# Kernel tuning notes

Measured on AMD Instinct MI355X. Metric: run time of the kernel, lower is better.

Reference implementation:

```python
import math
import jax, jax.numpy as jnp
import numpy as np

B, T, C = 2, 2048, 1024
H, N1, N2, N3 = 16, 6, 4, 6
HD = C // H  # 64


def setup_inputs() -> dict:
    key = jax.random.key(0)
    k1, k2, k3 = jax.random.split(key, 3)
    return {
        "x": jax.random.normal(k1, (B, T, C), jnp.float32),
        "qkv_w": jax.random.normal(k2, (3 * C, C), jnp.float32) * (C ** -0.5),
        "proj_w": jax.random.normal(k3, (C, C), jnp.float32) * (C ** -0.5),
        "proj_b": jnp.zeros((C,), jnp.float32),
        "curvature": jnp.ones((1, N2, 1, 1), jnp.float32),
    }


def _rotary(T_, hd, dtype):
    inv_freq = 1.0 / (10000.0 ** (jnp.arange(0, hd, 2, dtype=jnp.float32) / hd))
    freqs = jnp.outer(jnp.arange(T_, dtype=jnp.float32), inv_freq)  # [T, hd/2]
    return jnp.cos(freqs)[None, :, None, :].astype(dtype), jnp.sin(freqs)[None, :, None, :].astype(dtype)


def _apply_rot(x, cos, sin):
    x1, x2 = x[..., : x.shape[-1] // 2], x[..., x.shape[-1] // 2 :]
    return jnp.concatenate([x1 * cos + x2 * sin, -x1 * sin + x2 * cos], axis=-1).astype(x.dtype)


def _causal_bias(L, S, dtype):
    mask = jnp.triu(jnp.ones((L, S), bool), k=1)
    return jnp.where(mask, jnp.asarray(-jnp.inf, dtype), jnp.asarray(0.0, dtype))


def _sdpa(q, k, v, scale):
    # q,k,v: [B,h,T,hd]
    scores = jnp.einsum("bhtd,bhsd->bhts", q, k) * scale + _causal_bias(q.shape[-2], k.shape[-2], q.dtype)
    return jnp.einsum("bhts,bhsd->bhtd", jax.nn.softmax(scores, axis=-1), v)


def _hyp_attn(q, k, v, curv):
    # Lorentz-model hyperbolic attention. project(x,k) = [sqrt(1/k+||x||^2), x];
    # d(u,v) = sqrt(1/k) * arccosh(-k * <u,v>_L), <u,v>_L = -u0 v0 + <u_s, v_s>.
    eps = 1e-6
    tq = jnp.sqrt(1.0 / curv + jnp.sum(q * q, axis=-1, keepdims=True))  # [B,h,T,1]
    tk = jnp.sqrt(1.0 / curv + jnp.sum(k * k, axis=-1, keepdims=True))  # [B,h,S,1]
    inner = jnp.einsum("bhtd,bhsd->bhts", q, k) - tq * jnp.swapaxes(tk, -1, -2)  # Lorentz inner [B,h,T,S]
    arg = jnp.maximum(-curv * inner, 1.0 + 1e-7)
    dis = jnp.sqrt(1.0 / curv) * jnp.arccosh(arg)
    scores = 1.0 / (eps + dis) + _causal_bias(q.shape[-2], k.shape[-2], q.dtype)
    return jnp.einsum("bhts,bhsd->bhtd", jax.nn.softmax(scores, axis=-1), v)


def reference(x, qkv_w, proj_w, proj_b, curvature):
    Bx, Tx, Cx = x.shape
    qkv = x @ qkv_w.T  # [B,T,3C]
    q, k, v = jnp.split(qkv, 3, axis=-1)
    q = q.reshape(Bx, Tx, H, HD)
    k = k.reshape(Bx, Tx, H, HD)
    v = v.reshape(Bx, Tx, H, HD)
    cos, sin = _rotary(Tx, HD, x.dtype)
    q = _apply_rot(q, cos, sin)
    k = _apply_rot(k, cos, sin)
    # -> [B,H,T,hd]
    q, k, v = (jnp.swapaxes(t, 1, 2) for t in (q, k, v))
    outs = []
    # euclidean heads
    outs.append(_sdpa(q[:, :N1], k[:, :N1], v[:, :N1], 1.0 / math.sqrt(HD)))
    # hyperbolic heads
    outs.append(_hyp_attn(q[:, N1 : N1 + N2], k[:, N1 : N1 + N2], v[:, N1 : N1 + N2], curvature))
    # spherical heads (cosine-sim attention, scale = sqrt(head_dim))
    qn = q[:, N1 + N2 :] / jnp.maximum(jnp.linalg.norm(q[:, N1 + N2 :], axis=-1, keepdims=True), 1e-12)
    kn = k[:, N1 + N2 :] / jnp.maximum(jnp.linalg.norm(k[:, N1 + N2 :], axis=-1, keepdims=True), 1e-12)
    outs.append(_sdpa(qn, kn, v[:, N1 + N2 :], math.sqrt(HD)))
    y = jnp.concatenate(outs, axis=1)  # [B,H,T,hd]
    y = jnp.swapaxes(y, 1, 2).reshape(Bx, Tx, Cx)
    return y @ proj_w.T + proj_b
```

## Files before the change

kernel.cpp:

```cpp
#include <hip/hip_runtime.h>
#include <stdint.h>
#include <math.h>


typedef __bf16 bf16x8 __attribute__((ext_vector_type(8)));
typedef float f32x4 __attribute__((ext_vector_type(4)));

static __device__ __forceinline__ float bf2f(unsigned short u) {
  union { unsigned int i; float f; } v; v.i = ((unsigned int)u) << 16; return v.f;
}
static __device__ __forceinline__ unsigned short f2bf(float f) {
  union { float f; unsigned int i; } v; v.f = f;
  unsigned int x = v.i;
  x += 0x7fffu + ((x >> 16) & 1u);
  return (unsigned short)(x >> 16);
}

static __device__ __forceinline__ void async_copy16(const void* gsrc, void* ldst) {
  auto* lp = reinterpret_cast<__attribute__((address_space(3))) unsigned int*>(
      reinterpret_cast<uintptr_t>(ldst));
  auto* gp = reinterpret_cast<const __attribute__((address_space(1))) unsigned int*>(
      reinterpret_cast<uintptr_t>(gsrc));
  __builtin_amdgcn_global_load_lds(gp, lp, 16, 0, 0);
}

template <int PAT>
__global__ __launch_bounds__(256) void split2(const float* __restrict__ in,
                                              unsigned short* __restrict__ out) {
  const int row = blockIdx.x;
  const int kq = threadIdx.x * 4;
  const f32x4 x = *(const f32x4*)(in + (size_t)row * 1024 + kq);
  unsigned short hi[4], lo[4];
#pragma unroll
  for (int i = 0; i < 4; ++i) {
    hi[i] = f2bf(x[i]);
    lo[i] = f2bf(x[i] - bf2f(hi[i]));
  }
  uint2 uh, ul;
  uh.x = (unsigned)hi[0] | ((unsigned)hi[1] << 16);
  uh.y = (unsigned)hi[2] | ((unsigned)hi[3] << 16);
  ul.x = (unsigned)lo[0] | ((unsigned)lo[1] << 16);
  ul.y = (unsigned)lo[2] | ((unsigned)lo[3] << 16);
  unsigned short* op = out + (size_t)row * 2048 + kq;
  *(uint2*)(op)        = uh;
  *(uint2*)(op + 1024) = PAT ? uh : ul;
}

template <int HASBIAS>
__global__ __launch_bounds__(256) void gemm_bt(
    const unsigned short* __restrict__ A, const unsigned short* __restrict__ Bm,
    float* __restrict__ C, const float* __restrict__ bias, int N_, int K_) {
  alignas(16) __shared__ unsigned short smA[128 * 64];
  alignas(16) __shared__ unsigned short smB[128 * 64];
  const int tid = threadIdx.x;
  const int lane = tid & 63;
  const int wv = tid >> 6;
  const int wm = wv >> 1, wn = wv & 1;
  const long m0 = (long)blockIdx.y * 128, n0 = (long)blockIdx.x * 128;

  const f32x4 zero4 = {0.f, 0.f, 0.f, 0.f};
  f32x4 acc[4][4];
#pragma unroll
  for (int i = 0; i < 4; ++i)
#pragma unroll
    for (int j = 0; j < 4; ++j) acc[i][j] = zero4;

  int mrow[4], gg[4];
#pragma unroll
  for (int w = 0; w < 4; ++w) {
    int c = w * 256 + tid;
    mrow[w] = c >> 3;
    gg[w] = (c & 7) ^ ((c >> 3) & 7);
  }

  const int kTiles = K_ >> 6;
  for (int kt = 0; kt < kTiles; ++kt) {
    if (kt) __syncthreads();
    const int kb = kt << 6;
#pragma unroll
    for (int w = 0; w < 4; ++w) {
      const int c = w * 256 + tid;
      async_copy16(A + (size_t)(m0 + mrow[w]) * K_ + kb + gg[w] * 8,
                   (char*)smA + c * 16);
      async_copy16(Bm + (size_t)(n0 + mrow[w]) * K_ + kb + gg[w] * 8,
                   (char*)smB + c * 16);
    }
    __syncthreads();
#pragma unroll
    for (int ks = 0; ks < 2; ++ks) {
      bf16x8 af[4], bg[4];
#pragma unroll
      for (int i = 0; i < 4; ++i) {
        const int ra = wm * 64 + i * 16 + (lane & 15);
        const int ga = (ks * 4 + (lane >> 4)) ^ (ra & 7);
        af[i] = *(const bf16x8*)((const char*)smA + ra * 128 + ga * 16);
        const int rb = wn * 64 + i * 16 + (lane & 15);
        const int gb2 = (ks * 4 + (lane >> 4)) ^ (rb & 7);
        bg[i] = *(const bf16x8*)((const char*)smB + rb * 128 + gb2 * 16);
      }
#pragma unroll
      for (int i = 0; i < 4; ++i)
#pragma unroll
        for (int j = 0; j < 4; ++j)
          acc[i][j] = __builtin_amdgcn_mfma_f32_16x16x32_bf16(af[i], bg[j], acc[i][j], 0, 0, 0);
    }
  }

  const int r0 = wm * 64 + (lane >> 4) * 4;
  const int c0 = wn * 64 + (lane & 15);
#pragma unroll
  for (int j = 0; j < 4; ++j) {
    const long col = n0 + c0 + j * 16;
    float bv = 0.f;
    if (HASBIAS) bv = bias[col];
#pragma unroll
    for (int i = 0; i < 4; ++i) {
#pragma unroll
      for (int r = 0; r < 4; ++r) {
        const long row = m0 + r0 + i * 16 + r;
        C[row * N_ + col] = acc[i][j][r] + bv;
      }
    }
  }
}

__global__ __launch_bounds__(256) void prep(
    const float* __restrict__ qkvf, unsigned short* __restrict__ Q2,
    unsigned short* __restrict__ K2, unsigned short* __restrict__ V2,
    float* __restrict__ qq, float* __restrict__ kk, const float* __restrict__ curvg) {
  __shared__ unsigned short Vl[64 * 66];
  const int tid = threadIdx.x;
  const int zz = blockIdx.x;
  const int ttile = zz & 31, bh = zz >> 5;
  const int b = bh >> 4, h = bh & 15;
  const int t0 = ttile * 64;
  const int tr = tid >> 2, seg = tid & 3;
  const int t = t0 + tr;
  const float* src = qkvf + ((size_t)(b * 2048 + t)) * 3072 + h * 64 + seg * 16;

  float qv[16], kv[16], vv[16];
#pragma unroll
  for (int c = 0; c < 4; ++c) {
    const f32x4 a  = *(const f32x4*)(src + c * 4);
    const f32x4 bb = *(const f32x4*)(src + 1024 + c * 4);
    const f32x4 cc = *(const f32x4*)(src + 2048 + c * 4);
#pragma unroll
    for (int e = 0; e < 4; ++e) { qv[c*4+e] = a[e]; kv[c*4+e] = bb[e]; vv[c*4+e] = cc[e]; }
  }
  float qr[16], kr[16];
#pragma unroll
  for (int e = 0; e < 16; ++e) {
    const int d = seg * 16 + e;
    const int i = d & 31;
    const float invf = exp2f(-0.41524101186109286f * (float)i);
    float sn, cs;
    sincosf((float)t * invf, &sn, &cs);
    const float qo = __shfl_xor(qv[e], 2, 64);
    const float ko = __shfl_xor(kv[e], 2, 64);
    qr[e] = (d < 32) ? (qv[e] * cs + qo * sn) : (qv[e] * cs - qo * sn);
    kr[e] = (d < 32) ? (kv[e] * cs + ko * sn) : (kv[e] * cs - ko * sn);
  }
  float sq = 0.f, sk = 0.f;
#pragma unroll
  for (int e = 0; e < 16; ++e) { sq += qr[e] * qr[e]; sk += kr[e] * kr[e]; }
  sq += __shfl_xor(sq, 1, 64); sq += __shfl_xor(sq, 2, 64);
  sk += __shfl_xor(sk, 1, 64); sk += __shfl_xor(sk, 2, 64);
  float qscale = 0.125f * 1.4426950408889634f;
  if (h >= 10) {
    const float rq = 1.0f / fmaxf(sqrtf(sq), 1e-12f);
    const float rk = 1.0f / fmaxf(sqrtf(sk), 1e-12f);
#pragma unroll
    for (int e = 0; e < 16; ++e) { qr[e] *= rq; kr[e] *= rk; }
    qscale = 8.0f * 1.4426950408889634f;
  } else if (h >= 6) {
    qscale = 1.0f;
  }
#pragma unroll
  for (int e = 0; e < 16; ++e) qr[e] *= qscale;
  if (seg == 0) {
    const int idx = b * 32768 + h * 2048 + t;
    float oq = sq, ok = sk;
    if (h >= 6 && h < 10) {
      const float invc = 1.0f / curvg[h - 6];
      oq = sqrtf(invc + sq);
      ok = sqrtf(invc + sk);
    }
    qq[idx] = oq;
    kk[idx] = ok;
  }
  const int st = seg >> 1;
  const int quadA = (seg * 2) & 3, quadB = (seg * 2 + 1) & 3;
  {
    unsigned int wh[8], wl[8];
#pragma unroll
    for (int p = 0; p < 8; ++p) {
      unsigned short h0 = f2bf(qr[2*p]), h1 = f2bf(qr[2*p+1]);
      unsigned short l0 = f2bf(qr[2*p] - bf2f(h0)), l1 = f2bf(qr[2*p+1] - bf2f(h1));
      wh[p] = (unsigned)h0 | ((unsigned)h1 << 16);
      wl[p] = (unsigned)l0 | ((unsigned)l1 << 16);
    }
    const int qi = (t >> 4) & 1, c15q = t & 15;
    unsigned short* qs = Q2 + ((size_t)bh * 64 + (t >> 5)) * 4096;
    const int fh = ((qi * 2 + st) * 2 + 0) * 512, fl = fh + 512;
    *(uint4*)(qs + fh + quadA * 128 + c15q * 8) = uint4{wh[0], wh[1], wh[2], wh[3]};
    *(uint4*)(qs + fh + quadB * 128 + c15q * 8) = uint4{wh[4], wh[5], wh[6], wh[7]};
    *(uint4*)(qs + fl + quadA * 128 + c15q * 8) = uint4{wl[0], wl[1], wl[2], wl[3]};
    *(uint4*)(qs + fl + quadB * 128 + c15q * 8) = uint4{wl[4], wl[5], wl[6], wl[7]};
#pragma unroll
    for (int p = 0; p < 8; ++p) {
      unsigned short h0 = f2bf(kr[2*p]), h1 = f2bf(kr[2*p+1]);
      wh[p] = (unsigned)h0 | ((unsigned)h1 << 16);
    }
    const int kj = (tr >> 4) & 3, c15k = tr & 15;
    unsigned short* ks = K2 + ((size_t)bh * 32 + ttile) * 4096;
    const int gh = (st * 4 + kj) * 512;
    *(uint4*)(ks + gh + quadA * 128 + c15k * 8) = uint4{wh[0], wh[1], wh[2], wh[3]};
    *(uint4*)(ks + gh + quadB * 128 + c15k * 8) = uint4{wh[4], wh[5], wh[6], wh[7]};
  }
#pragma unroll
  for (int e = 0; e < 16; ++e) Vl[(seg * 16 + e) * 66 + tr] = f2bf(vv[e]);
  __syncthreads();
  {
    const int d = tid >> 2, tch = (tid & 3) * 16;
    unsigned int wv2[8];
#pragma unroll
    for (int p = 0; p < 8; ++p) {
      const unsigned short a0 = Vl[d * 66 + tch + 2*p];
      const unsigned short a1 = Vl[d * 66 + tch + 2*p + 1];
      wv2[p] = (unsigned)a0 | ((unsigned)a1 << 16);
    }
    const int dj = d >> 4, c15v = d & 15;
    const int ks2 = tch >> 5;
    const int qvA = (tch >> 3) & 3, qvB = ((tch >> 3) + 1) & 3;
    unsigned short* vs = V2 + ((size_t)bh * 32 + ttile) * 4096 + (ks2 * 4 + dj) * 512;
    *(uint4*)(vs + qvA * 128 + c15v * 8) = uint4{wv2[0], wv2[1], wv2[2], wv2[3]};
    *(uint4*)(vs + qvB * 128 + c15v * 8) = uint4{wv2[4], wv2[5], wv2[6], wv2[7]};
  }
}

__global__ __launch_bounds__(256, 2) void attn_part(
    const unsigned short* __restrict__ Q2, const unsigned short* __restrict__ K2,
    const unsigned short* __restrict__ V2, const float* __restrict__ tqq,
    const float* __restrict__ tkk, const float* __restrict__ curvg,
    float* __restrict__ part) {
  alignas(16) __shared__ unsigned short Pl[4][32 * 64];
  const int tid = threadIdx.x;
  const int lane = tid & 63;
  const int wv = tid >> 6;
  unsigned short* Pw = &Pl[wv][0];
  const int quad = lane >> 4, c15 = lane & 15;
  const int z = blockIdx.x * 4 + wv;
  const int bh = z / 160;
  const int u = 159 - (z - bh * 160);
  int qw, ch;
  if (u < 16)      { qw = u; ch = 0; }
  else if (u < 48) { qw = 16 + ((u - 16) >> 1); ch = (u - 16) & 1; }
  else if (u < 96) { const int s2 = u - 48; const int q3 = s2 / 3; qw = 32 + q3; ch = s2 - 3 * q3; }
  else             { const int s2 = u - 96; qw = 48 + (s2 >> 2); ch = s2 & 3; }
  const int h = bh & 15;
  const int geom = (h < 6) ? 0 : ((h < 10) ? 1 : 2);
  const int qrow0 = qw * 32;
  const f32x4 zero4 = {0.f, 0.f, 0.f, 0.f};

  const unsigned short* qbase = Q2 + ((size_t)bh * 64 + qw) * 4096;
  bf16x8 qh[2][2], ql[2][2];
#pragma unroll
  for (int qi = 0; qi < 2; ++qi)
#pragma unroll
    for (int st = 0; st < 2; ++st) {
      const int f = ((qi * 2 + st) * 2) * 512 + lane * 8;
      qh[qi][st] = *(const bf16x8*)(qbase + f);
      ql[qi][st] = *(const bf16x8*)(qbase + f + 512);
    }

  float curv = 1.f, sic = 1.f;
  const float Moff = 4.0f;
  f32x4 tq4[2] = {zero4, zero4};
  if (geom == 1) {
    curv = curvg[h - 6];
    sic = sqrtf(1.0f / curv);
#pragma unroll
    for (int qi = 0; qi < 2; ++qi)
      tq4[qi] = *(const f32x4*)(tqq + bh * 2048 + qrow0 + qi * 16 + quad * 4);
  }

  const __bf16 one_b = (__bf16)1.0f;
  const bf16x8 ones = {one_b, one_b, one_b, one_b, one_b, one_b, one_b, one_b};

  f32x4 o[2][4];
  f32x4 ol[2] = {zero4, zero4};
#pragma unroll
  for (int qi = 0; qi < 2; ++qi)
#pragma unroll
    for (int dj = 0; dj < 4; ++dj) o[qi][dj] = zero4;

  const int nkt = (qw >> 1) + 1;
  const int ktB = ch * 8;
  const int ktE = (ktB + 8 < nkt) ? (ktB + 8) : nkt;
  for (int kt = ktB; kt < ktE; ++kt) {
    const int kb = kt * 64;
    const unsigned short* kbase = K2 + ((size_t)bh * 32 + kt) * 4096;
    const unsigned short* vbase = V2 + ((size_t)bh * 32 + kt) * 4096;

    bf16x8 kf[2][4], vf[2][4];
#pragma unroll
    for (int st = 0; st < 2; ++st)
#pragma unroll
      for (int kj = 0; kj < 4; ++kj)
        kf[st][kj] = *(const bf16x8*)(kbase + (st * 4 + kj) * 512 + lane * 8);
#pragma unroll
    for (int ks2 = 0; ks2 < 2; ++ks2)
#pragma unroll
      for (int dj = 0; dj < 4; ++dj)
        vf[ks2][dj] = *(const bf16x8*)(vbase + (ks2 * 4 + dj) * 512 + lane * 8);
    float tkf[4];
    if (geom == 1) {
#pragma unroll
      for (int kj = 0; kj < 4; ++kj)
        tkf[kj] = tkk[bh * 2048 + kb + kj * 16 + c15];
    }

    f32x4 s[2][4];
#pragma unroll
    for (int qi = 0; qi < 2; ++qi)
#pragma unroll
      for (int kj = 0; kj < 4; ++kj) s[qi][kj] = zero4;
    __builtin_amdgcn_s_setprio(1);
#pragma unroll
    for (int st = 0; st < 2; ++st) {
#pragma unroll
      for (int kj = 0; kj < 4; ++kj) {
#pragma unroll
        for (int qi = 0; qi < 2; ++qi) {
          s[qi][kj] = __builtin_amdgcn_mfma_f32_16x16x32_bf16(qh[qi][st], kf[st][kj], s[qi][kj], 0, 0, 0);
          s[qi][kj] = __builtin_amdgcn_mfma_f32_16x16x32_bf16(ql[qi][st], kf[st][kj], s[qi][kj], 0, 0, 0);
        }
      }
    }
    __builtin_amdgcn_s_setprio(0);

    const bool needmask = (kt == nkt - 1);
#pragma unroll
    for (int qi = 0; qi < 2; ++qi) {
      const int qbaserow = qrow0 + qi * 16 + quad * 4;
#pragma unroll
      for (int kj = 0; kj < 4; ++kj) {
        const int skey = kj * 16 + c15;
        const int key = kb + skey;
        const f32x4 d4 = s[qi][kj];
        f32x4 p;
        if (geom == 1) {
          const float tk = tkf[kj];
#pragma unroll
          for (int r = 0; r < 4; ++r) {
            const float a = fmaxf(curv * (tq4[qi][r] * tk - d4[r]), 1.0f + 1e-7f);
            const float dis = sic * __logf(a + sqrtf(a * a - 1.0f));
            p[r] = __expf(__builtin_amdgcn_rcpf(1e-6f + dis) - Moff);
          }
        } else {
#pragma unroll
          for (int r = 0; r < 4; ++r) p[r] = exp2f(d4[r]);
        }
        if (needmask) {
#pragma unroll
          for (int r = 0; r < 4; ++r)
            if (key > qbaserow + r) p[r] = 0.0f;
        }
#pragma unroll
        for (int r = 0; r < 4; ++r) {
          union { float f; unsigned u2; } pv; pv.f = p[r];
          const int row = qi * 16 + quad * 4 + r;
          const int g = (skey >> 3) ^ (row & 7);
          Pw[row * 64 + g * 8 + (skey & 7)] = (unsigned short)(pv.u2 >> 16);
        }
      }
    }

    __builtin_amdgcn_s_setprio(1);
#pragma unroll
    for (int ks2 = 0; ks2 < 2; ++ks2) {
      bf16x8 av[2];
#pragma unroll
      for (int qi = 0; qi < 2; ++qi) {
        const int m = qi * 16 + c15;
        const int g = (ks2 * 4 + quad) ^ (m & 7);
        av[qi] = *(const bf16x8*)(Pw + m * 64 + g * 8);
        ol[qi] = __builtin_amdgcn_mfma_f32_16x16x32_bf16(av[qi], ones, ol[qi], 0, 0, 0);
      }
#pragma unroll
      for (int dj = 0; dj < 4; ++dj) {
#pragma unroll
        for (int qi = 0; qi < 2; ++qi)
          o[qi][dj] = __builtin_amdgcn_mfma_f32_16x16x32_bf16(av[qi], vf[ks2][dj], o[qi][dj], 0, 0, 0);
      }
    }
    __builtin_amdgcn_s_setprio(0);
  }

  float* slot = part + (size_t)(bh * 160 + u) * 2112;
#pragma unroll
  for (int qi = 0; qi < 2; ++qi)
#pragma unroll
    for (int dj = 0; dj < 4; ++dj)
      *(f32x4*)(slot + (qi * 4 + dj) * 256 + lane * 4) = o[qi][dj];
  if (c15 == 0) {
#pragma unroll
    for (int qi = 0; qi < 2; ++qi)
      *(f32x4*)(slot + 2048 + qi * 16 + quad * 4) = ol[qi];
  }
}

__global__ __launch_bounds__(256) void attn_reduce(
    const float* __restrict__ part, unsigned short* __restrict__ Ay) {
  __shared__ float Ol[4][32 * 65];
  const int tid = threadIdx.x;
  const int lane = tid & 63;
  const int wv = tid >> 6;
  float* Olw = &Ol[wv][0];
  const int quad = lane >> 4, c15 = lane & 15;
  const int z = blockIdx.x * 4 + wv, bh = z & 31, qw = 63 - (z >> 5);
  const int b = bh >> 4, h = bh & 15;
  const int G = qw >> 4;
  const int base = qw + 8 * G * (G - 1) + (qw & 15) * G;
  const float* slot0 = part + (size_t)(bh * 160 + base) * 2112;

  const f32x4 zero4 = {0.f, 0.f, 0.f, 0.f};
  f32x4 o[8];
  f32x4 l4[2] = {zero4, zero4};
#pragma unroll
  for (int i = 0; i < 8; ++i) o[i] = zero4;
  for (int chv = 0; chv <= G; ++chv) {
    const float* sl = slot0 + chv * 2112;
#pragma unroll
    for (int i = 0; i < 8; ++i) o[i] += *(const f32x4*)(sl + i * 256 + lane * 4);
#pragma unroll
    for (int qi = 0; qi < 2; ++qi)
      l4[qi] += *(const f32x4*)(sl + 2048 + qi * 16 + quad * 4);
  }
#pragma unroll
  for (int qi = 0; qi < 2; ++qi) {
    f32x4 invl;
#pragma unroll
    for (int r = 0; r < 4; ++r) invl[r] = __builtin_amdgcn_rcpf(l4[qi][r]);
#pragma unroll
    for (int dj = 0; dj < 4; ++dj) {
      const f32x4 val = o[qi * 4 + dj] * invl;
#pragma unroll
      for (int r = 0; r < 4; ++r)
        Olw[(qi * 16 + quad * 4 + r) * 65 + dj * 16 + c15] = val[r];
    }
  }
  __syncthreads();
  const int row = lane >> 1, half = lane & 1;
  const float* rp = Olw + row * 65 + half * 32;
  unsigned int uh[16], ul2[16];
#pragma unroll
  for (int p = 0; p < 16; ++p) {
    const float v0 = rp[2 * p], v1 = rp[2 * p + 1];
    const unsigned short h0 = f2bf(v0), h1 = f2bf(v1);
    const unsigned short g0 = f2bf(v0 - bf2f(h0)), g1 = f2bf(v1 - bf2f(h1));
    uh[p] = (unsigned)h0 | ((unsigned)h1 << 16);
    ul2[p] = (unsigned)g0 | ((unsigned)g1 << 16);
  }
  unsigned short* yp = Ay + ((size_t)(b * 2048 + qw * 32 + row)) * 2048 + h * 64 + half * 32;
#pragma unroll
  for (int c = 0; c < 4; ++c) {
    *(uint4*)(yp + 8 * c)        = uint4{uh[4*c], uh[4*c+1], uh[4*c+2], uh[4*c+3]};
    *(uint4*)(yp + 1024 + 8 * c) = uint4{ul2[4*c], ul2[4*c+1], ul2[4*c+2], ul2[4*c+3]};
  }
}

extern "C" void kernel_launch(void* const* d_in, const int* in_sizes, int n_in,
                              void* d_out, int out_size, void* d_ws, size_t ws_size,
                              hipStream_t stream) {
  const float* x      = (const float*)d_in[0];
  const float* qkv_w  = (const float*)d_in[1];
  const float* proj_w = (const float*)d_in[2];
  const float* proj_b = (const float*)d_in[3];
  const float* curvature = (const float*)d_in[4];
  float* out = (float*)d_out;

  char* ws = (char*)d_ws;
  unsigned short* AX   = (unsigned short*)ws;
  unsigned short* BW   = (unsigned short*)(ws + 16777216);
  float*          QKVF = (float*)(ws + 33554432);
  unsigned short* Q2   = (unsigned short*)ws;
  unsigned short* K2   = (unsigned short*)(ws + 16777216);
  unsigned short* V2   = (unsigned short*)(ws + 25165824);
  float*          PART = (float*)(ws + 33554432);
  unsigned short* BPW  = (unsigned short*)(ws + 76808192);
  unsigned short* AY   = (unsigned short*)ws;
  float*          QQ   = (float*)(ws + 94371840);
  float*          KK   = (float*)(ws + 94633984);

  split2<0><<<4096, 256, 0, stream>>>(x, AX);
  split2<1><<<3072, 256, 0, stream>>>(qkv_w, BW);

  gemm_bt<0><<<dim3(24, 32), 256, 0, stream>>>(AX, BW, QKVF, nullptr, 3072, 2048);

  prep<<<1024, 256, 0, stream>>>(QKVF, Q2, K2, V2, QQ, KK, curvature);

  split2<1><<<1024, 256, 0, stream>>>(proj_w, BPW);

  attn_part<<<1280, 256, 0, stream>>>(Q2, K2, V2, QQ, KK, curvature, PART);

  attn_reduce<<<512, 256, 0, stream>>>(PART, AY);

  gemm_bt<1><<<dim3(8, 32), 256, 0, stream>>>(AY, BPW, out, proj_b, 1024, 2048);
}
```

Baseline: 286.7 us.

## Transpose score MFMAs and pass P via ds_bpermute instead of LDS

Swaps the MFMA operand order so scores come out transposed (keys along rows, queries along lanes). The probability tile can then be packed into registers and redistributed with ds_bpermute as the B operand of the PV MFMA, instead of a scatter-store to shared memory and a read-back. Downstream indexing for tq/tk, the causal mask, row-sum output and the reduce kernel's layout are adjusted to match. It removes the per-wave LDS P buffer and its strided 2-byte stores, but adds 16 bpermutes and selects per tile.

After: 285.2 us. About the same (-0.5%).

```diff
diff --git a/kernel.cpp b/kernel.cpp
--- a/kernel.cpp
+++ b/kernel.cpp
@@ -243,11 +243,9 @@
     const unsigned short* __restrict__ V2, const float* __restrict__ tqq,
     const float* __restrict__ tkk, const float* __restrict__ curvg,
     float* __restrict__ part) {
-  alignas(16) __shared__ unsigned short Pl[4][32 * 64];
   const int tid = threadIdx.x;
   const int lane = tid & 63;
   const int wv = tid >> 6;
-  unsigned short* Pw = &Pl[wv][0];
   const int quad = lane >> 4, c15 = lane & 15;
   const int z = blockIdx.x * 4 + wv;
   const int bh = z / 160;
@@ -275,17 +273,21 @@
 
   float curv = 1.f, sic = 1.f;
   const float Moff = 4.0f;
-  f32x4 tq4[2] = {zero4, zero4};
+  float tqs[2] = {0.f, 0.f};
   if (geom == 1) {
     curv = curvg[h - 6];
     sic = sqrtf(1.0f / curv);
 #pragma unroll
     for (int qi = 0; qi < 2; ++qi)
-      tq4[qi] = *(const f32x4*)(tqq + bh * 2048 + qrow0 + qi * 16 + quad * 4);
+      tqs[qi] = tqq[bh * 2048 + qrow0 + qi * 16 + c15];
   }
 
   const __bf16 one_b = (__bf16)1.0f;
   const bf16x8 ones = {one_b, one_b, one_b, one_b, one_b, one_b, one_b, one_b};
+
+  const int iA = ((quad & 1) * 32 + c15) * 4;
+  const int iB = iA + 64;
+  const bool hiq = (quad >= 2);
 
   f32x4 o[2][4];
   f32x4 ol[2] = {zero4, zero4};
@@ -313,11 +315,11 @@
 #pragma unroll
       for (int dj = 0; dj < 4; ++dj)
         vf[ks2][dj] = *(const bf16x8*)(vbase + (ks2 * 4 + dj) * 512 + lane * 8);
-    float tkf[4];
+    f32x4 tk4[4];
     if (geom == 1) {
 #pragma unroll
       for (int kj = 0; kj < 4; ++kj)
-        tkf[kj] = tkk[bh * 2048 + kb + kj * 16 + c15];
+        tk4[kj] = *(const f32x4*)(tkk + bh * 2048 + kb + kj * 16 + quad * 4);
     }
 
     f32x4 s[2][4];
@@ -332,28 +334,28 @@
       for (int kj = 0; kj < 4; ++kj) {
 #pragma unroll
         for (int qi = 0; qi < 2; ++qi) {
-          s[qi][kj] = __builtin_amdgcn_mfma_f32_16x16x32_bf16(qh[qi][st], kf[st][kj], s[qi][kj], 0, 0, 0);
-          s[qi][kj] = __builtin_amdgcn_mfma_f32_16x16x32_bf16(ql[qi][st], kf[st][kj], s[qi][kj], 0, 0, 0);
+          s[qi][kj] = __builtin_amdgcn_mfma_f32_16x16x32_bf16(kf[st][kj], qh[qi][st], s[qi][kj], 0, 0, 0);
+          s[qi][kj] = __builtin_amdgcn_mfma_f32_16x16x32_bf16(kf[st][kj], ql[qi][st], s[qi][kj], 0, 0, 0);
         }
       }
     }
     __builtin_amdgcn_s_setprio(0);
 
     const bool needmask = (kt == nkt - 1);
+    unsigned pw[2][4][2];
 #pragma unroll
     for (int qi = 0; qi < 2; ++qi) {
-      const int qbaserow = qrow0 + qi * 16 + quad * 4;
+      const int qcol = qrow0 + qi * 16 + c15;
 #pragma unroll
       for (int kj = 0; kj < 4; ++kj) {
-        const int skey = kj * 16 + c15;
-        const int key = kb + skey;
+        const int kloc = kb + kj * 16 + quad * 4;
         const f32x4 d4 = s[qi][kj];
         f32x4 p;
         if (geom == 1) {
-          const float tk = tkf[kj];
+          const float tq = tqs[qi];
 #pragma unroll
           for (int r = 0; r < 4; ++r) {
-            const float a = fmaxf(curv * (tq4[qi][r] * tk - d4[r]), 1.0f + 1e-7f);
+            const float a = fmaxf(curv * (tq * tk4[kj][r] - d4[r]), 1.0f + 1e-7f);
             const float dis = sic * __logf(a + sqrtf(a * a - 1.0f));
             p[r] = __expf(__builtin_amdgcn_rcpf(1e-6f + dis) - Moff);
           }
@@ -364,34 +366,39 @@
         if (needmask) {
 #pragma unroll
           for (int r = 0; r < 4; ++r)
-            if (key > qbaserow + r) p[r] = 0.0f;
+            if (kloc + r > qcol) p[r] = 0.0f;
         }
-#pragma unroll
-        for (int r = 0; r < 4; ++r) {
-          union { float f; unsigned u2; } pv; pv.f = p[r];
-          const int row = qi * 16 + quad * 4 + r;
-          const int g = (skey >> 3) ^ (row & 7);
-          Pw[row * 64 + g * 8 + (skey & 7)] = (unsigned short)(pv.u2 >> 16);
-        }
+        union { float f; unsigned u2; } b0, b1, b2, b3;
+        b0.f = p[0]; b1.f = p[1]; b2.f = p[2]; b3.f = p[3];
+        pw[qi][kj][0] = (b0.u2 >> 16) | (b1.u2 & 0xffff0000u);
+        pw[qi][kj][1] = (b2.u2 >> 16) | (b3.u2 & 0xffff0000u);
       }
     }
 
     __builtin_amdgcn_s_setprio(1);
 #pragma unroll
     for (int ks2 = 0; ks2 < 2; ++ks2) {
-      bf16x8 av[2];
+      const int a = ks2 * 2, b2 = ks2 * 2 + 1;
 #pragma unroll
       for (int qi = 0; qi < 2; ++qi) {
-        const int m = qi * 16 + c15;
-        const int g = (ks2 * 4 + quad) ^ (m & 7);
-        av[qi] = *(const bf16x8*)(Pw + m * 64 + g * 8);
-        ol[qi] = __builtin_amdgcn_mfma_f32_16x16x32_bf16(av[qi], ones, ol[qi], 0, 0, 0);
-      }
-#pragma unroll
-      for (int dj = 0; dj < 4; ++dj) {
-#pragma unroll
-        for (int qi = 0; qi < 2; ++qi)
-          o[qi][dj] = __builtin_amdgcn_mfma_f32_16x16x32_bf16(av[qi], vf[ks2][dj], o[qi][dj], 0, 0, 0);
+        const int w0A = __builtin_amdgcn_ds_bpermute(iA, (int)pw[qi][a][0]);
+        const int w0B = __builtin_amdgcn_ds_bpermute(iA, (int)pw[qi][b2][0]);
+        const int w1A = __builtin_amdgcn_ds_bpermute(iA, (int)pw[qi][a][1]);
+        const int w1B = __builtin_amdgcn_ds_bpermute(iA, (int)pw[qi][b2][1]);
+        const int w2A = __builtin_amdgcn_ds_bpermute(iB, (int)pw[qi][a][0]);
+        const int w2B = __builtin_amdgcn_ds_bpermute(iB, (int)pw[qi][b2][0]);
+        const int w3A = __builtin_amdgcn_ds_bpermute(iB, (int)pw[qi][a][1]);
+        const int w3B = __builtin_amdgcn_ds_bpermute(iB, (int)pw[qi][b2][1]);
+        union { uint4 u; bf16x8 v; } pf;
+        pf.u.x = (unsigned)(hiq ? w0B : w0A);
+        pf.u.y = (unsigned)(hiq ? w1B : w1A);
+        pf.u.z = (unsigned)(hiq ? w2B : w2A);
+        pf.u.w = (unsigned)(hiq ? w3B : w3A);
+        const bf16x8 pfrag = pf.v;
+        ol[qi] = __builtin_amdgcn_mfma_f32_16x16x32_bf16(ones, pfrag, ol[qi], 0, 0, 0);
+#pragma unroll
+        for (int dj = 0; dj < 4; ++dj)
+          o[qi][dj] = __builtin_amdgcn_mfma_f32_16x16x32_bf16(vf[ks2][dj], pfrag, o[qi][dj], 0, 0, 0);
       }
     }
     __builtin_amdgcn_s_setprio(0);
@@ -403,10 +410,10 @@
 #pragma unroll
     for (int dj = 0; dj < 4; ++dj)
       *(f32x4*)(slot + (qi * 4 + dj) * 256 + lane * 4) = o[qi][dj];
-  if (c15 == 0) {
+  if (quad == 0) {
 #pragma unroll
     for (int qi = 0; qi < 2; ++qi)
-      *(f32x4*)(slot + 2048 + qi * 16 + quad * 4) = ol[qi];
+      slot[2048 + qi * 16 + c15] = ol[qi][0];
   }
 }
 
@@ -426,7 +433,7 @@
 
   const f32x4 zero4 = {0.f, 0.f, 0.f, 0.f};
   f32x4 o[8];
-  f32x4 l4[2] = {zero4, zero4};
+  float ls[2] = {0.f, 0.f};
 #pragma unroll
   for (int i = 0; i < 8; ++i) o[i] = zero4;
   for (int chv = 0; chv <= G; ++chv) {
@@ -435,19 +442,17 @@
     for (int i = 0; i < 8; ++i) o[i] += *(const f32x4*)(sl + i * 256 + lane * 4);
 #pragma unroll
     for (int qi = 0; qi < 2; ++qi)
-      l4[qi] += *(const f32x4*)(sl + 2048 + qi * 16 + quad * 4);
+      ls[qi] += sl[2048 + qi * 16 + c15];
   }
 #pragma unroll
   for (int qi = 0; qi < 2; ++qi) {
-    f32x4 invl;
-#pragma unroll
-    for (int r = 0; r < 4; ++r) invl[r] = __builtin_amdgcn_rcpf(l4[qi][r]);
+    const float invl = __builtin_amdgcn_rcpf(ls[qi]);
 #pragma unroll
     for (int dj = 0; dj < 4; ++dj) {
       const f32x4 val = o[qi * 4 + dj] * invl;
 #pragma unroll
       for (int r = 0; r < 4; ++r)
-        Olw[(qi * 16 + quad * 4 + r) * 65 + dj * 16 + c15] = val[r];
+        Olw[(qi * 16 + c15) * 65 + dj * 16 + quad * 4 + r] = val[r];
     }
   }
   __syncthreads();
```
